# Kernel tuning notes

Hardware: AMD Instinct MI355X
Metric: run time of the kernel (lower is better)

Reference implementation:

```python
import jax, jax.numpy as jnp
import numpy as np

NQ, NKV, D = 32, 8, 64
HID = 2048
EPS = 1e-5
THETA = 1000000.0


def _rmsnorm(x, w):
    var = jnp.mean(x * x, axis=-1, keepdims=True)
    return x * jax.lax.rsqrt(var + EPS) * w


def setup_inputs() -> dict:
    key = jax.random.key(0)
    k1, k2, k3 = jax.random.split(key, 3)
    T = 2048
    positions = jnp.arange(T, dtype=jnp.int64) if jax.config.jax_enable_x64 else jnp.arange(T, dtype=jnp.int32)
    hidden_states = jax.random.normal(k1, (T, HID), dtype=jnp.float32)
    w_qkv = jax.random.normal(k2, (HID, (NQ + 2 * NKV) * D), dtype=jnp.float32) / np.sqrt(HID)
    w_out = jax.random.normal(k3, (NQ * D, HID), dtype=jnp.float32) / np.sqrt(NQ * D)
    q_ln_w = jnp.ones((D,), dtype=jnp.float32)
    k_ln_w = jnp.ones((D,), dtype=jnp.float32)
    return {"positions": positions, "hidden_states": hidden_states, "w_qkv": w_qkv,
            "w_out": w_out, "q_ln_w": q_ln_w, "k_ln_w": k_ln_w}


def reference(positions, hidden_states, w_qkv, w_out, q_ln_w, k_ln_w):
    T = hidden_states.shape[0]
    qkv = hidden_states @ w_qkv  # [T, (NQ+2*NKV)*D]
    q = qkv[:, : NQ * D].reshape(T, NQ, D)
    k = qkv[:, NQ * D : (NQ + NKV) * D].reshape(T, NKV, D)
    v = qkv[:, (NQ + NKV) * D :].reshape(T, NKV, D)
    # per-head RMSNorm on q and k
    q = _rmsnorm(q, q_ln_w)
    k = _rmsnorm(k, k_ln_w)
    # neox-style RoPE (rotate halves)
    inv_freq = 1.0 / (THETA ** (jnp.arange(0, D, 2, dtype=jnp.float32) / D))
    ang = positions.astype(jnp.float32)[:, None] * inv_freq  # [T, D/2]
    cos = jnp.cos(ang)[:, None, :]
    sin = jnp.sin(ang)[:, None, :]
    def rope(x):
        x1, x2 = x[..., : D // 2], x[..., D // 2 :]
        return jnp.concatenate([x1 * cos - x2 * sin, x2 * cos + x1 * sin], axis=-1)
    q = rope(q)
    k = rope(k)
    # grouped-query causal attention (one sequence, positions define order)
    G = NQ // NKV
    qg = q.reshape(T, NKV, G, D)
    scores = jnp.einsum('tkgd,skd->kgts', qg, k) * (D ** -0.5)  # [NKV,G,T,T]
    causal = jnp.arange(T)[:, None] >= jnp.arange(T)[None, :]
    scores = jnp.where(causal[None, None], scores, -1e30)
    probs = jax.nn.softmax(scores, axis=-1)
    attn = jnp.einsum('kgts,skd->tkgd', probs, v).reshape(T, NQ * D)
    return attn @ w_out
```

## Files before the change

### kernel.cpp

```cpp
#include <hip/hip_runtime.h>

typedef __bf16 bhalf;
typedef __bf16 bhalf8 __attribute__((ext_vector_type(8)));
typedef __bf16 bhalf4 __attribute__((ext_vector_type(4)));
typedef float f32x4 __attribute__((ext_vector_type(4)));

typedef __attribute__((address_space(1))) const void* gas_p;
typedef __attribute__((address_space(3))) void* las_p;

#define T_SEQ 2048
#define HIDN  2048
#define NQH   32
#define NKVH  8
#define DH    64
#define NQKV  3072

__global__ __launch_bounds__(256) void cast_bf16_k(const float* __restrict__ in,
                                                   bhalf* __restrict__ out, int n) {
  int i = (blockIdx.x * 256 + threadIdx.x) * 4;
  if (i + 3 < n) {
    float4 v = *(const float4*)(in + i);
    bhalf4 o;
    o[0] = (bhalf)v.x; o[1] = (bhalf)v.y; o[2] = (bhalf)v.z; o[3] = (bhalf)v.w;
    *(bhalf4*)(out + i) = o;
  }
}

__global__ __launch_bounds__(256) void transpose_cast64_k(const float* __restrict__ in,
                                                          bhalf* __restrict__ out,
                                                          int R, int C) {
  __shared__ bhalf tile[64][72];
  int tid = threadIdx.x;
  int bx = blockIdx.x * 64;
  int by = blockIdx.y * 64;
  int rl = tid >> 4, c4 = (tid & 15) * 4;
#pragma unroll
  for (int p = 0; p < 4; ++p) {
    float4 v = *(const float4*)(in + (size_t)(by + rl + 16 * p) * C + bx + c4);
    bhalf4 b;
    b[0] = (bhalf)v.x; b[1] = (bhalf)v.y; b[2] = (bhalf)v.z; b[3] = (bhalf)v.w;
    *(bhalf4*)&tile[rl + 16 * p][c4] = b;
  }
  __syncthreads();
  int c = tid >> 2, r0 = (tid & 3) * 16;
  bhalf8 o0, o1;
#pragma unroll
  for (int j = 0; j < 8; ++j) { o0[j] = tile[r0 + j][c]; o1[j] = tile[r0 + 8 + j][c]; }
  *(bhalf8*)(out + (size_t)(bx + c) * R + by + r0) = o0;
  *(bhalf8*)(out + (size_t)(bx + c) * R + by + r0 + 8) = o1;
}

__device__ __forceinline__ void gemm_core64(const bhalf* __restrict__ A,
                                            const bhalf* __restrict__ Bt,
                                            int Kstride, int Klen,
                                            int bm, int bn, int tid,
                                            bhalf* As, bhalf* Bs, f32x4 acc[4]) {
  int lane = tid & 63, wv = tid >> 6;
  int m16 = lane & 15, q4 = lane >> 4;
  int srow = tid >> 3;
  int scol = ((tid & 7) ^ (srow & 7)) * 8;
  const bhalf* asrc = A + (size_t)(bm + srow) * Kstride + scol;
  const bhalf* bsrc = Bt + (size_t)(bn + srow) * Kstride + scol;
  bhalf* adst = As + (wv * 8) * 64;
  bhalf* bdst = Bs + (wv * 8) * 64;
  int swz = m16 & 7;

  for (int k0 = 0; k0 < Klen; k0 += 64) {
#pragma unroll
    for (int c = 0; c < 2; ++c) {
      __builtin_amdgcn_global_load_lds((gas_p)(asrc + (size_t)(c * 32) * Kstride + k0),
                                       (las_p)(adst + c * 2048), 16, 0, 0);
      __builtin_amdgcn_global_load_lds((gas_p)(bsrc + (size_t)(c * 32) * Kstride + k0),
                                       (las_p)(bdst + c * 2048), 16, 0, 0);
    }
    __syncthreads();
    bhalf8 af[2], bf[4][2];
#pragma unroll
    for (int ks = 0; ks < 2; ++ks)
      af[ks] = *(const bhalf8*)&As[(wv * 16 + m16) * 64 + (((ks * 4 + q4) ^ swz) * 8)];
#pragma unroll
    for (int ni = 0; ni < 4; ++ni)
#pragma unroll
      for (int ks = 0; ks < 2; ++ks)
        bf[ni][ks] = *(const bhalf8*)&Bs[(ni * 16 + m16) * 64 + (((ks * 4 + q4) ^ swz) * 8)];
#pragma unroll
    for (int ni = 0; ni < 4; ++ni) {
      acc[ni] = __builtin_amdgcn_mfma_f32_16x16x32_bf16(af[0], bf[ni][0], acc[ni], 0, 0, 0);
      acc[ni] = __builtin_amdgcn_mfma_f32_16x16x32_bf16(af[1], bf[ni][1], acc[ni], 0, 0, 0);
    }
    __syncthreads();
  }
}

__global__ __launch_bounds__(256) void gemm1_fused_k(const bhalf* __restrict__ A,
                                                     const bhalf* __restrict__ Bt,
                                                     const int* __restrict__ pos,
                                                     const float* __restrict__ qw,
                                                     const float* __restrict__ kw,
                                                     bhalf* __restrict__ qo,
                                                     bhalf* __restrict__ ko,
                                                     bhalf* __restrict__ vt) {
  __shared__ __align__(16) bhalf As[64 * 64];
  __shared__ __align__(16) bhalf Bs[64 * 64];
  int tid = threadIdx.x, lane = tid & 63, wv = tid >> 6;
  int m16 = lane & 15, q4 = lane >> 4;
  int bm = blockIdx.y * 64, bn = blockIdx.x * 64, h = blockIdx.x;
  f32x4 zero4 = {0.f, 0.f, 0.f, 0.f};
  f32x4 acc[4];
#pragma unroll
  for (int ni = 0; ni < 4; ++ni) acc[ni] = zero4;

  gemm_core64(A, Bt, HIDN, HIDN, bm, bn, tid, As, Bs, acc);

  if (h < 40) {
    float wd[4];
    const float* wptr = (h < 32) ? qw : kw;
#pragma unroll
    for (int ni = 0; ni < 4; ++ni) wd[ni] = wptr[ni * 16 + m16];
    float f0 = exp2f((float)m16 * -0.6228615177913804f);
    float f1 = f0 * 0.001f;
#pragma unroll
    for (int r = 0; r < 4; ++r) {
      int trow = bm + wv * 16 + q4 * 4 + r;
      float x0 = acc[0][r], x1 = acc[1][r], x2 = acc[2][r], x3 = acc[3][r];
      float ss = x0 * x0 + x1 * x1 + x2 * x2 + x3 * x3;
      ss += __shfl_xor(ss, 1);
      ss += __shfl_xor(ss, 2);
      ss += __shfl_xor(ss, 4);
      ss += __shfl_xor(ss, 8);
      float sc = rsqrtf(ss * (1.0f / 64.0f) + 1e-5f);
      float y0 = x0 * sc * wd[0], y1 = x1 * sc * wd[1];
      float y2 = x2 * sc * wd[2], y3 = x3 * sc * wd[3];
      float p = (float)pos[trow];
      float a0 = p * f0, a1 = p * f1;
      float c0 = cosf(a0), s0 = sinf(a0), c1 = cosf(a1), s1 = sinf(a1);
      float o0 = y0 * c0 - y2 * s0, o2 = y2 * c0 + y0 * s0;
      float o1 = y1 * c1 - y3 * s1, o3 = y3 * c1 + y1 * s1;
      bhalf* dst = (h < 32) ? (qo + (size_t)trow * 2048 + h * 64 + m16)
                            : (ko + (size_t)trow * 512 + (h - 32) * 64 + m16);
      dst[0] = (bhalf)o0; dst[16] = (bhalf)o1; dst[32] = (bhalf)o2; dst[48] = (bhalf)o3;
    }
  } else {
#pragma unroll
    for (int r = 0; r < 4; ++r) {
      int trow = bm + wv * 16 + q4 * 4 + r;
#pragma unroll
      for (int ni = 0; ni < 4; ++ni)
        vt[(size_t)((h - 40) * 64 + ni * 16 + m16) * 2048 + trow] = (bhalf)acc[ni][r];
    }
  }
}

__global__ __launch_bounds__(256) void gemm2_k(const bhalf* __restrict__ A,
                                               const bhalf* __restrict__ Bt,
                                               float* __restrict__ Cpart) {
  __shared__ __align__(16) bhalf As[64 * 64];
  __shared__ __align__(16) bhalf Bs[64 * 64];
  int tid = threadIdx.x, lane = tid & 63, wv = tid >> 6;
  int m16 = lane & 15, q4 = lane >> 4;
  int bm = blockIdx.y * 64, bn = blockIdx.x * 64;
  int slice = blockIdx.z;
  f32x4 zero4 = {0.f, 0.f, 0.f, 0.f};
  f32x4 acc[4];
#pragma unroll
  for (int ni = 0; ni < 4; ++ni) acc[ni] = zero4;

  gemm_core64(A + slice * 1024, Bt + slice * 1024, HIDN, 1024, bm, bn, tid, As, Bs, acc);

  float* C = Cpart + (size_t)slice * (T_SEQ * HIDN);
#pragma unroll
  for (int r = 0; r < 4; ++r) {
    size_t base = (size_t)(bm + wv * 16 + q4 * 4 + r) * 2048 + bn + m16;
    C[base] = acc[0][r]; C[base + 16] = acc[1][r];
    C[base + 32] = acc[2][r]; C[base + 48] = acc[3][r];
  }
}

__global__ __launch_bounds__(256) void add2_k(const float* __restrict__ p0,
                                              const float* __restrict__ p1,
                                              float* __restrict__ out) {
  int i = (blockIdx.x * 256 + threadIdx.x) * 4;
  float4 a = *(const float4*)(p0 + i);
  float4 b = *(const float4*)(p1 + i);
  float4 o = {a.x + b.x, a.y + b.y, a.z + b.z, a.w + b.w};
  *(float4*)(out + i) = o;
}

__global__ __launch_bounds__(256) void attn_k(const bhalf* __restrict__ q,
                                              const bhalf* __restrict__ k,
                                              const bhalf* __restrict__ vt,
                                              bhalf* __restrict__ o) {
  __shared__ __align__(16) bhalf Kb[2][4096];
  __shared__ __align__(16) bhalf Vb[2][4096];
  __shared__ __align__(16) bhalf Pb[4][16][72];
  int tid = threadIdx.x, lane = tid & 63, w = tid >> 6;
  int h = blockIdx.x, kh = h >> 2;
  int qt = 31 - blockIdx.y;
  int qb = qt * 64;
  int m16 = lane & 15, q4 = lane >> 4;
  int wrow0 = qb + w * 16;

  const float C1 = 0.18033688011112042f;
  const float C2 = 11.541560327111707f;

  const bhalf* qp = q + (size_t)(wrow0 + m16) * 2048 + h * 64;
  bhalf8 qf0 = *(const bhalf8*)(qp + q4 * 8);
  bhalf8 qf1 = *(const bhalf8*)(qp + 32 + q4 * 8);

  int srow = tid >> 3;
  int scol = ((tid & 7) ^ (srow & 7)) * 8;
  const bhalf* ksrc = k + (size_t)srow * 512 + kh * 64 + scol;
  const bhalf* vsrc = vt + (size_t)(kh * 64 + srow) * 2048 + scol;
  bhalf* kdst = &Kb[0][0] + w * 512;
  bhalf* vdst = &Vb[0][0] + w * 512;

  auto stage = [&](int c) {
    int buf = c & 1, s0 = c * 64;
#pragma unroll
    for (int j = 0; j < 2; ++j) {
      __builtin_amdgcn_global_load_lds((gas_p)(ksrc + (size_t)(s0 + j * 32) * 512),
                                       (las_p)(kdst + buf * 4096 + j * 2048), 16, 0, 0);
      __builtin_amdgcn_global_load_lds((gas_p)(vsrc + (size_t)(j * 32) * 2048 + s0),
                                       (las_p)(vdst + buf * 4096 + j * 2048), 16, 0, 0);
    }
  };

  f32x4 zero4 = {0.f, 0.f, 0.f, 0.f};
  f32x4 oac[4];
  float psum[4] = {0.f, 0.f, 0.f, 0.f};
#pragma unroll
  for (int ni = 0; ni < 4; ++ni) oac[ni] = zero4;
  int swz = m16 & 7;

  stage(0);
  for (int c = 0; c <= qt; ++c) {
    __syncthreads();
    if (c < qt) stage(c + 1);
    int buf = c & 1, s0 = c * 64;
    if (c < qt) {
      bhalf8 kf[4][2];
#pragma unroll
      for (int st = 0; st < 4; ++st)
#pragma unroll
        for (int ks = 0; ks < 2; ++ks)
          kf[st][ks] = *(const bhalf8*)&Kb[buf][(st * 16 + m16) * 64 + (((ks * 4 + q4) ^ swz) * 8)];
      f32x4 sv[4];
#pragma unroll
      for (int st = 0; st < 4; ++st) {
        f32x4 t0 = __builtin_amdgcn_mfma_f32_16x16x32_bf16(qf0, kf[st][0], zero4, 0, 0, 0);
        sv[st] = __builtin_amdgcn_mfma_f32_16x16x32_bf16(qf1, kf[st][1], t0, 0, 0, 0);
      }
#pragma unroll
      for (int st = 0; st < 4; ++st)
#pragma unroll
        for (int r = 0; r < 4; ++r) {
          float pe = exp2f(sv[st][r] * C1 - C2);
          psum[r] += pe;
          Pb[w][q4 * 4 + r][st * 16 + m16] = (bhalf)pe;
        }
      bhalf8 vf[4][2];
#pragma unroll
      for (int ni = 0; ni < 4; ++ni)
#pragma unroll
        for (int ks = 0; ks < 2; ++ks)
          vf[ni][ks] = *(const bhalf8*)&Vb[buf][(ni * 16 + m16) * 64 + (((ks * 4 + q4) ^ swz) * 8)];
      bhalf8 ap0 = *(const bhalf8*)&Pb[w][m16][q4 * 8];
      bhalf8 ap1 = *(const bhalf8*)&Pb[w][m16][32 + q4 * 8];
#pragma unroll
      for (int ni = 0; ni < 4; ++ni) {
        oac[ni] = __builtin_amdgcn_mfma_f32_16x16x32_bf16(ap0, vf[ni][0], oac[ni], 0, 0, 0);
        oac[ni] = __builtin_amdgcn_mfma_f32_16x16x32_bf16(ap1, vf[ni][1], oac[ni], 0, 0, 0);
      }
    } else {
      bhalf8 kf[4][2];
      f32x4 sv[4];
#pragma unroll
      for (int st = 0; st < 4; ++st)
        if (st <= w) {
#pragma unroll
          for (int ks = 0; ks < 2; ++ks)
            kf[st][ks] = *(const bhalf8*)&Kb[buf][(st * 16 + m16) * 64 + (((ks * 4 + q4) ^ swz) * 8)];
          f32x4 t0 = __builtin_amdgcn_mfma_f32_16x16x32_bf16(qf0, kf[st][0], zero4, 0, 0, 0);
          sv[st] = __builtin_amdgcn_mfma_f32_16x16x32_bf16(qf1, kf[st][1], t0, 0, 0, 0);
        }
      int stwr = (w >= 2) ? 3 : 1;
#pragma unroll
      for (int st = 0; st < 4; ++st) {
        if (st > stwr) continue;
#pragma unroll
        for (int r = 0; r < 4; ++r) {
          float pe = 0.f;
          if (st <= w) {
            int trow = wrow0 + q4 * 4 + r;
            int col = s0 + st * 16 + m16;
            pe = (col <= trow) ? exp2f(sv[st][r] * C1 - C2) : 0.f;
          }
          psum[r] += pe;
          Pb[w][q4 * 4 + r][st * 16 + m16] = (bhalf)pe;
        }
      }
      int ksmax = (w >= 2) ? 1 : 0;
      bhalf8 vf[4][2];
#pragma unroll
      for (int ni = 0; ni < 4; ++ni)
#pragma unroll
        for (int ks = 0; ks < 2; ++ks)
          if (ks <= ksmax)
            vf[ni][ks] = *(const bhalf8*)&Vb[buf][(ni * 16 + m16) * 64 + (((ks * 4 + q4) ^ swz) * 8)];
      bhalf8 ap0 = *(const bhalf8*)&Pb[w][m16][q4 * 8];
#pragma unroll
      for (int ni = 0; ni < 4; ++ni)
        oac[ni] = __builtin_amdgcn_mfma_f32_16x16x32_bf16(ap0, vf[ni][0], oac[ni], 0, 0, 0);
      if (ksmax) {
        bhalf8 ap1 = *(const bhalf8*)&Pb[w][m16][32 + q4 * 8];
#pragma unroll
        for (int ni = 0; ni < 4; ++ni)
          oac[ni] = __builtin_amdgcn_mfma_f32_16x16x32_bf16(ap1, vf[ni][1], oac[ni], 0, 0, 0);
      }
    }
  }
#pragma unroll
  for (int r = 0; r < 4; ++r) {
    float ps = psum[r];
    ps += __shfl_xor(ps, 1);
    ps += __shfl_xor(ps, 2);
    ps += __shfl_xor(ps, 4);
    ps += __shfl_xor(ps, 8);
    psum[r] = 1.0f / ps;
  }
#pragma unroll
  for (int ni = 0; ni < 4; ++ni)
#pragma unroll
    for (int r = 0; r < 4; ++r) {
      int trow = wrow0 + q4 * 4 + r;
      o[(size_t)trow * 2048 + h * 64 + ni * 16 + m16] = (bhalf)(oac[ni][r] * psum[r]);
    }
}

extern "C" void kernel_launch(void* const* d_in, const int* in_sizes, int n_in,
                              void* d_out, int out_size, void* d_ws, size_t ws_size,
                              hipStream_t stream) {
  const int* positions = (const int*)d_in[0];
  const float* hidden  = (const float*)d_in[1];
  const float* w_qkv   = (const float*)d_in[2];
  const float* w_out   = (const float*)d_in[3];
  const float* q_ln    = (const float*)d_in[4];
  const float* k_ln    = (const float*)d_in[5];
  float* out = (float*)d_out;

  char* wsp = (char*)d_ws;
  bhalf* woutT   = (bhalf*)(wsp);
  bhalf* attn_bf = (bhalf*)(wsp + 8388608);
  float* part0   = (float*)(wsp + 16777216);
  float* part1   = (float*)(wsp + 33554432);
  bhalf* hid_bf  = (bhalf*)(wsp + 16777216);
  bhalf* wqkvT   = (bhalf*)(wsp + 25165824);
  bhalf* q_bf    = (bhalf*)(wsp + 50331648);
  bhalf* k_bf    = (bhalf*)(wsp + 58720256);
  bhalf* vt_g    = (bhalf*)(wsp + 60817408);

  cast_bf16_k<<<T_SEQ * HIDN / 1024, 256, 0, stream>>>(hidden, hid_bf, T_SEQ * HIDN);
  transpose_cast64_k<<<dim3(NQKV / 64, HIDN / 64), 256, 0, stream>>>(w_qkv, wqkvT, HIDN, NQKV);
  transpose_cast64_k<<<dim3(HIDN / 64, HIDN / 64), 256, 0, stream>>>(w_out, woutT, HIDN, HIDN);
  gemm1_fused_k<<<dim3(NQKV / 64, T_SEQ / 64), 256, 0, stream>>>(
      hid_bf, wqkvT, positions, q_ln, k_ln, q_bf, k_bf, vt_g);
  attn_k<<<dim3(NQH, 32), 256, 0, stream>>>(q_bf, k_bf, vt_g, attn_bf);
  gemm2_k<<<dim3(HIDN / 64, T_SEQ / 64, 2), 256, 0, stream>>>(attn_bf, woutT, part0);
  add2_k<<<T_SEQ * HIDN / 1024, 256, 0, stream>>>(part0, part1, out);
}
```

Baseline: 237.9 us.

## Double-buffer GEMM LDS tiles and grow M tile to 128 rows

The shared GEMM core now double-buffers the LDS tiles. It issues the async global-to-LDS loads for the next K step before computing the current one, which removes one barrier per iteration and overlaps memory traffic with MFMA work. Each block also covers 128 rows instead of 64, so each wave computes a 32x64 sub-tile that reuses its B fragments across two A fragments, and both GEMM grids are halved to match. This raises LDS use to 48 KB and doubles the accumulator registers, which may lower occupancy and halves the block count on a GPU with many CUs.

Result: faster. 233.0 us (-2.0%).

```diff
diff --git a/kernel.cpp b/kernel.cpp
--- a/kernel.cpp
+++ b/kernel.cpp
@@ -50,11 +50,11 @@
   *(bhalf8*)(out + (size_t)(bx + c) * R + by + r0 + 8) = o1;
 }
 
-__device__ __forceinline__ void gemm_core64(const bhalf* __restrict__ A,
-                                            const bhalf* __restrict__ Bt,
-                                            int Kstride, int Klen,
-                                            int bm, int bn, int tid,
-                                            bhalf* As, bhalf* Bs, f32x4 acc[4]) {
+__device__ __forceinline__ void gemm_core_db(const bhalf* __restrict__ A,
+                                             const bhalf* __restrict__ Bt,
+                                             int Kstride, int Klen,
+                                             int bm, int bn, int tid,
+                                             bhalf* As, bhalf* Bs, f32x4 acc[2][4]) {
   int lane = tid & 63, wv = tid >> 6;
   int m16 = lane & 15, q4 = lane >> 4;
   int srow = tid >> 3;
@@ -64,31 +64,46 @@
   bhalf* adst = As + (wv * 8) * 64;
   bhalf* bdst = Bs + (wv * 8) * 64;
   int swz = m16 & 7;
-
-  for (int k0 = 0; k0 < Klen; k0 += 64) {
-#pragma unroll
-    for (int c = 0; c < 2; ++c) {
+  int nit = Klen >> 6;
+
+  auto stage = [&](int it) {
+    int buf = it & 1, k0 = it * 64;
+#pragma unroll
+    for (int c = 0; c < 4; ++c)
       __builtin_amdgcn_global_load_lds((gas_p)(asrc + (size_t)(c * 32) * Kstride + k0),
-                                       (las_p)(adst + c * 2048), 16, 0, 0);
+                                       (las_p)(adst + buf * 8192 + c * 2048), 16, 0, 0);
+#pragma unroll
+    for (int c = 0; c < 2; ++c)
       __builtin_amdgcn_global_load_lds((gas_p)(bsrc + (size_t)(c * 32) * Kstride + k0),
-                                       (las_p)(bdst + c * 2048), 16, 0, 0);
-    }
+                                       (las_p)(bdst + buf * 4096 + c * 2048), 16, 0, 0);
+  };
+
+  stage(0);
+  for (int it = 0; it < nit; ++it) {
     __syncthreads();
-    bhalf8 af[2], bf[4][2];
-#pragma unroll
-    for (int ks = 0; ks < 2; ++ks)
-      af[ks] = *(const bhalf8*)&As[(wv * 16 + m16) * 64 + (((ks * 4 + q4) ^ swz) * 8)];
+    if (it + 1 < nit) stage(it + 1);
+    const bhalf* Ab = As + (it & 1) * 8192;
+    const bhalf* Bb = Bs + (it & 1) * 4096;
+    bhalf8 af[2][2], bf[4][2];
+#pragma unroll
+    for (int mi = 0; mi < 2; ++mi)
+#pragma unroll
+      for (int ks = 0; ks < 2; ++ks)
+        af[mi][ks] = *(const bhalf8*)&Ab[(wv * 32 + mi * 16 + m16) * 64 +
+                                         (((ks * 4 + q4) ^ swz) * 8)];
 #pragma unroll
     for (int ni = 0; ni < 4; ++ni)
 #pragma unroll
       for (int ks = 0; ks < 2; ++ks)
-        bf[ni][ks] = *(const bhalf8*)&Bs[(ni * 16 + m16) * 64 + (((ks * 4 + q4) ^ swz) * 8)];
-#pragma unroll
-    for (int ni = 0; ni < 4; ++ni) {
-      acc[ni] = __builtin_amdgcn_mfma_f32_16x16x32_bf16(af[0], bf[ni][0], acc[ni], 0, 0, 0);
-      acc[ni] = __builtin_amdgcn_mfma_f32_16x16x32_bf16(af[1], bf[ni][1], acc[ni], 0, 0, 0);
-    }
-    __syncthreads();
+        bf[ni][ks] = *(const bhalf8*)&Bb[(ni * 16 + m16) * 64 +
+                                         (((ks * 4 + q4) ^ swz) * 8)];
+#pragma unroll
+    for (int mi = 0; mi < 2; ++mi)
+#pragma unroll
+      for (int ni = 0; ni < 4; ++ni) {
+        acc[mi][ni] = __builtin_amdgcn_mfma_f32_16x16x32_bf16(af[mi][0], bf[ni][0], acc[mi][ni], 0, 0, 0);
+        acc[mi][ni] = __builtin_amdgcn_mfma_f32_16x16x32_bf16(af[mi][1], bf[ni][1], acc[mi][ni], 0, 0, 0);
+      }
   }
 }
 
@@ -100,17 +115,19 @@
                                                      bhalf* __restrict__ qo,
                                                      bhalf* __restrict__ ko,
                                                      bhalf* __restrict__ vt) {
-  __shared__ __align__(16) bhalf As[64 * 64];
-  __shared__ __align__(16) bhalf Bs[64 * 64];
+  __shared__ __align__(16) bhalf As[2 * 128 * 64];
+  __shared__ __align__(16) bhalf Bs[2 * 64 * 64];
   int tid = threadIdx.x, lane = tid & 63, wv = tid >> 6;
   int m16 = lane & 15, q4 = lane >> 4;
-  int bm = blockIdx.y * 64, bn = blockIdx.x * 64, h = blockIdx.x;
+  int bm = blockIdx.y * 128, bn = blockIdx.x * 64, h = blockIdx.x;
   f32x4 zero4 = {0.f, 0.f, 0.f, 0.f};
-  f32x4 acc[4];
-#pragma unroll
-  for (int ni = 0; ni < 4; ++ni) acc[ni] = zero4;
-
-  gemm_core64(A, Bt, HIDN, HIDN, bm, bn, tid, As, Bs, acc);
+  f32x4 acc[2][4];
+#pragma unroll
+  for (int mi = 0; mi < 2; ++mi)
+#pragma unroll
+    for (int ni = 0; ni < 4; ++ni) acc[mi][ni] = zero4;
+
+  gemm_core_db(A, Bt, HIDN, HIDN, bm, bn, tid, As, Bs, acc);
 
   if (h < 40) {
     float wd[4];
@@ -120,60 +137,68 @@
     float f0 = exp2f((float)m16 * -0.6228615177913804f);
     float f1 = f0 * 0.001f;
 #pragma unroll
-    for (int r = 0; r < 4; ++r) {
-      int trow = bm + wv * 16 + q4 * 4 + r;
-      float x0 = acc[0][r], x1 = acc[1][r], x2 = acc[2][r], x3 = acc[3][r];
-      float ss = x0 * x0 + x1 * x1 + x2 * x2 + x3 * x3;
-      ss += __shfl_xor(ss, 1);
-      ss += __shfl_xor(ss, 2);
-      ss += __shfl_xor(ss, 4);
-      ss += __shfl_xor(ss, 8);
-      float sc = rsqrtf(ss * (1.0f / 64.0f) + 1e-5f);
-      float y0 = x0 * sc * wd[0], y1 = x1 * sc * wd[1];
-      float y2 = x2 * sc * wd[2], y3 = x3 * sc * wd[3];
-      float p = (float)pos[trow];
-      float a0 = p * f0, a1 = p * f1;
-      float c0 = cosf(a0), s0 = sinf(a0), c1 = cosf(a1), s1 = sinf(a1);
-      float o0 = y0 * c0 - y2 * s0, o2 = y2 * c0 + y0 * s0;
-      float o1 = y1 * c1 - y3 * s1, o3 = y3 * c1 + y1 * s1;
-      bhalf* dst = (h < 32) ? (qo + (size_t)trow * 2048 + h * 64 + m16)
-                            : (ko + (size_t)trow * 512 + (h - 32) * 64 + m16);
-      dst[0] = (bhalf)o0; dst[16] = (bhalf)o1; dst[32] = (bhalf)o2; dst[48] = (bhalf)o3;
-    }
+    for (int mi = 0; mi < 2; ++mi)
+#pragma unroll
+      for (int r = 0; r < 4; ++r) {
+        int trow = bm + wv * 32 + mi * 16 + q4 * 4 + r;
+        float x0 = acc[mi][0][r], x1 = acc[mi][1][r], x2 = acc[mi][2][r], x3 = acc[mi][3][r];
+        float ss = x0 * x0 + x1 * x1 + x2 * x2 + x3 * x3;
+        ss += __shfl_xor(ss, 1);
+        ss += __shfl_xor(ss, 2);
+        ss += __shfl_xor(ss, 4);
+        ss += __shfl_xor(ss, 8);
+        float sc = rsqrtf(ss * (1.0f / 64.0f) + 1e-5f);
+        float y0 = x0 * sc * wd[0], y1 = x1 * sc * wd[1];
+        float y2 = x2 * sc * wd[2], y3 = x3 * sc * wd[3];
+        float p = (float)pos[trow];
+        float a0 = p * f0, a1 = p * f1;
+        float c0 = cosf(a0), s0 = sinf(a0), c1 = cosf(a1), s1 = sinf(a1);
+        float o0 = y0 * c0 - y2 * s0, o2 = y2 * c0 + y0 * s0;
+        float o1 = y1 * c1 - y3 * s1, o3 = y3 * c1 + y1 * s1;
+        bhalf* dst = (h < 32) ? (qo + (size_t)trow * 2048 + h * 64 + m16)
+                              : (ko + (size_t)trow * 512 + (h - 32) * 64 + m16);
+        dst[0] = (bhalf)o0; dst[16] = (bhalf)o1; dst[32] = (bhalf)o2; dst[48] = (bhalf)o3;
+      }
   } else {
 #pragma unroll
-    for (int r = 0; r < 4; ++r) {
-      int trow = bm + wv * 16 + q4 * 4 + r;
-#pragma unroll
-      for (int ni = 0; ni < 4; ++ni)
-        vt[(size_t)((h - 40) * 64 + ni * 16 + m16) * 2048 + trow] = (bhalf)acc[ni][r];
-    }
+    for (int mi = 0; mi < 2; ++mi)
+#pragma unroll
+      for (int r = 0; r < 4; ++r) {
+        int trow = bm + wv * 32 + mi * 16 + q4 * 4 + r;
+#pragma unroll
+        for (int ni = 0; ni < 4; ++ni)
+          vt[(size_t)((h - 40) * 64 + ni * 16 + m16) * 2048 + trow] = (bhalf)acc[mi][ni][r];
+      }
   }
 }
 
 __global__ __launch_bounds__(256) void gemm2_k(const bhalf* __restrict__ A,
                                                const bhalf* __restrict__ Bt,
                                                float* __restrict__ Cpart) {
-  __shared__ __align__(16) bhalf As[64 * 64];
-  __shared__ __align__(16) bhalf Bs[64 * 64];
+  __shared__ __align__(16) bhalf As[2 * 128 * 64];
+  __shared__ __align__(16) bhalf Bs[2 * 64 * 64];
   int tid = threadIdx.x, lane = tid & 63, wv = tid >> 6;
   int m16 = lane & 15, q4 = lane >> 4;
-  int bm = blockIdx.y * 64, bn = blockIdx.x * 64;
+  int bm = blockIdx.y * 128, bn = blockIdx.x * 64;
   int slice = blockIdx.z;
   f32x4 zero4 = {0.f, 0.f, 0.f, 0.f};
-  f32x4 acc[4];
-#pragma unroll
-  for (int ni = 0; ni < 4; ++ni) acc[ni] = zero4;
-
-  gemm_core64(A + slice * 1024, Bt + slice * 1024, HIDN, 1024, bm, bn, tid, As, Bs, acc);
+  f32x4 acc[2][4];
+#pragma unroll
+  for (int mi = 0; mi < 2; ++mi)
+#pragma unroll
+    for (int ni = 0; ni < 4; ++ni) acc[mi][ni] = zero4;
+
+  gemm_core_db(A + slice * 1024, Bt + slice * 1024, HIDN, 1024, bm, bn, tid, As, Bs, acc);
 
   float* C = Cpart + (size_t)slice * (T_SEQ * HIDN);
 #pragma unroll
-  for (int r = 0; r < 4; ++r) {
-    size_t base = (size_t)(bm + wv * 16 + q4 * 4 + r) * 2048 + bn + m16;
-    C[base] = acc[0][r]; C[base + 16] = acc[1][r];
-    C[base + 32] = acc[2][r]; C[base + 48] = acc[3][r];
-  }
+  for (int mi = 0; mi < 2; ++mi)
+#pragma unroll
+    for (int r = 0; r < 4; ++r) {
+      size_t base = (size_t)(bm + wv * 32 + mi * 16 + q4 * 4 + r) * 2048 + bn + m16;
+      C[base] = acc[mi][0][r]; C[base + 16] = acc[mi][1][r];
+      C[base + 32] = acc[mi][2][r]; C[base + 48] = acc[mi][3][r];
+    }
 }
 
 __global__ __launch_bounds__(256) void add2_k(const float* __restrict__ p0,
@@ -362,9 +387,9 @@
   cast_bf16_k<<<T_SEQ * HIDN / 1024, 256, 0, stream>>>(hidden, hid_bf, T_SEQ * HIDN);
   transpose_cast64_k<<<dim3(NQKV / 64, HIDN / 64), 256, 0, stream>>>(w_qkv, wqkvT, HIDN, NQKV);
   transpose_cast64_k<<<dim3(HIDN / 64, HIDN / 64), 256, 0, stream>>>(w_out, woutT, HIDN, HIDN);
-  gemm1_fused_k<<<dim3(NQKV / 64, T_SEQ / 64), 256, 0, stream>>>(
+  gemm1_fused_k<<<dim3(NQKV / 64, T_SEQ / 128), 256, 0, stream>>>(
       hid_bf, wqkvT, positions, q_ln, k_ln, q_bf, k_bf, vt_g);
   attn_k<<<dim3(NQH, 32), 256, 0, stream>>>(q_bf, k_bf, vt_g, attn_bf);
-  gemm2_k<<<dim3(HIDN / 64, T_SEQ / 64, 2), 256, 0, stream>>>(attn_bf, woutT, part0);
+  gemm2_k<<<dim3(HIDN / 64, T_SEQ / 128, 2), 256, 0, stream>>>(attn_bf, woutT, part0);
   add2_k<<<T_SEQ * HIDN / 1024, 256, 0, stream>>>(part0, part1, out);
 }
```

## Switch GEMMs to 32x32x16 MFMA with 64x128 tiles and fragment-ordered LDS

Applied to the files above, without the earlier changes.

Replaces the 16x16x32 MFMA GEMM core with a 32x32x16 variant. Each workgroup now computes a 64x128 tile, with each wave producing a 32x64 output. LDS is laid out in MFMA fragment order so each lane loads its fragment contiguously, which removes the XOR swizzle. The fused RMSNorm/RoPE epilogue and the output stores are rewritten for the 32x32 accumulator layout, where one head spans two accumulators per wave. The aim is fewer MFMA instructions and LDS reads per FLOP and better operand reuse, at the cost of fewer workgroups and higher register pressure.

Result: slower. 295.7 us (+24.3%).

```diff
diff --git a/kernel.cpp b/kernel.cpp
--- a/kernel.cpp
+++ b/kernel.cpp
@@ -4,6 +4,7 @@
 typedef __bf16 bhalf8 __attribute__((ext_vector_type(8)));
 typedef __bf16 bhalf4 __attribute__((ext_vector_type(4)));
 typedef float f32x4 __attribute__((ext_vector_type(4)));
+typedef float f32x16 __attribute__((ext_vector_type(16)));
 
 typedef __attribute__((address_space(1))) const void* gas_p;
 typedef __attribute__((address_space(3))) void* las_p;
@@ -50,43 +51,43 @@
   *(bhalf8*)(out + (size_t)(bx + c) * R + by + r0 + 8) = o1;
 }
 
-__device__ __forceinline__ void gemm_core64(const bhalf* __restrict__ A,
+__device__ __forceinline__ void gemm_core32(const bhalf* __restrict__ A,
                                             const bhalf* __restrict__ Bt,
-                                            int Kstride, int Klen,
-                                            int bm, int bn, int tid,
-                                            bhalf* As, bhalf* Bs, f32x4 acc[4]) {
+                                            int K, int Klen, int bm, int bn, int tid,
+                                            bhalf* As, bhalf* Bs, f32x16 acc[2]) {
   int lane = tid & 63, wv = tid >> 6;
-  int m16 = lane & 15, q4 = lane >> 4;
-  int srow = tid >> 3;
-  int scol = ((tid & 7) ^ (srow & 7)) * 8;
-  const bhalf* asrc = A + (size_t)(bm + srow) * Kstride + scol;
-  const bhalf* bsrc = Bt + (size_t)(bn + srow) * Kstride + scol;
-  bhalf* adst = As + (wv * 8) * 64;
-  bhalf* bdst = Bs + (wv * 8) * 64;
-  int swz = m16 & 7;
+  int r32 = lane & 31, khi = (lane >> 5) * 8;
+  const bhalf* ag[2];
+  const bhalf* bg[4];
+#pragma unroll
+  for (int i = 0; i < 2; ++i) {
+    int a = 2 * wv + i;
+    ag[i] = A + (size_t)(bm + (a >> 2) * 32 + r32) * K + (a & 3) * 16 + khi;
+  }
+#pragma unroll
+  for (int j = 0; j < 4; ++j) {
+    int b = 4 * wv + j;
+    bg[j] = Bt + (size_t)(bn + (b >> 2) * 32 + r32) * K + (b & 3) * 16 + khi;
+  }
+  bhalf* adst = As + (2 * wv) * 512;
+  bhalf* bdst = Bs + (4 * wv) * 512;
+  int mt = wv >> 1, ntb = (wv & 1) * 2;
 
   for (int k0 = 0; k0 < Klen; k0 += 64) {
 #pragma unroll
-    for (int c = 0; c < 2; ++c) {
-      __builtin_amdgcn_global_load_lds((gas_p)(asrc + (size_t)(c * 32) * Kstride + k0),
-                                       (las_p)(adst + c * 2048), 16, 0, 0);
-      __builtin_amdgcn_global_load_lds((gas_p)(bsrc + (size_t)(c * 32) * Kstride + k0),
-                                       (las_p)(bdst + c * 2048), 16, 0, 0);
-    }
+    for (int i = 0; i < 2; ++i)
+      __builtin_amdgcn_global_load_lds((gas_p)(ag[i] + k0), (las_p)(adst + i * 512), 16, 0, 0);
+#pragma unroll
+    for (int j = 0; j < 4; ++j)
+      __builtin_amdgcn_global_load_lds((gas_p)(bg[j] + k0), (las_p)(bdst + j * 512), 16, 0, 0);
     __syncthreads();
-    bhalf8 af[2], bf[4][2];
-#pragma unroll
-    for (int ks = 0; ks < 2; ++ks)
-      af[ks] = *(const bhalf8*)&As[(wv * 16 + m16) * 64 + (((ks * 4 + q4) ^ swz) * 8)];
-#pragma unroll
-    for (int ni = 0; ni < 4; ++ni)
-#pragma unroll
-      for (int ks = 0; ks < 2; ++ks)
-        bf[ni][ks] = *(const bhalf8*)&Bs[(ni * 16 + m16) * 64 + (((ks * 4 + q4) ^ swz) * 8)];
-#pragma unroll
-    for (int ni = 0; ni < 4; ++ni) {
-      acc[ni] = __builtin_amdgcn_mfma_f32_16x16x32_bf16(af[0], bf[ni][0], acc[ni], 0, 0, 0);
-      acc[ni] = __builtin_amdgcn_mfma_f32_16x16x32_bf16(af[1], bf[ni][1], acc[ni], 0, 0, 0);
+#pragma unroll
+    for (int ks = 0; ks < 4; ++ks) {
+      bhalf8 af  = *(const bhalf8*)&As[(mt * 4 + ks) * 512 + lane * 8];
+      bhalf8 bf0 = *(const bhalf8*)&Bs[(ntb * 4 + ks) * 512 + lane * 8];
+      bhalf8 bf1 = *(const bhalf8*)&Bs[((ntb + 1) * 4 + ks) * 512 + lane * 8];
+      acc[0] = __builtin_amdgcn_mfma_f32_32x32x16_bf16(af, bf0, acc[0], 0, 0, 0);
+      acc[1] = __builtin_amdgcn_mfma_f32_32x32x16_bf16(af, bf1, acc[1], 0, 0, 0);
     }
     __syncthreads();
   }
@@ -100,53 +101,55 @@
                                                      bhalf* __restrict__ qo,
                                                      bhalf* __restrict__ ko,
                                                      bhalf* __restrict__ vt) {
-  __shared__ __align__(16) bhalf As[64 * 64];
-  __shared__ __align__(16) bhalf Bs[64 * 64];
+  __shared__ __align__(16) bhalf As[8 * 512];
+  __shared__ __align__(16) bhalf Bs[16 * 512];
   int tid = threadIdx.x, lane = tid & 63, wv = tid >> 6;
-  int m16 = lane & 15, q4 = lane >> 4;
-  int bm = blockIdx.y * 64, bn = blockIdx.x * 64, h = blockIdx.x;
-  f32x4 zero4 = {0.f, 0.f, 0.f, 0.f};
-  f32x4 acc[4];
-#pragma unroll
-  for (int ni = 0; ni < 4; ++ni) acc[ni] = zero4;
-
-  gemm_core64(A, Bt, HIDN, HIDN, bm, bn, tid, As, Bs, acc);
-
-  if (h < 40) {
-    float wd[4];
-    const float* wptr = (h < 32) ? qw : kw;
-#pragma unroll
-    for (int ni = 0; ni < 4; ++ni) wd[ni] = wptr[ni * 16 + m16];
-    float f0 = exp2f((float)m16 * -0.6228615177913804f);
-    float f1 = f0 * 0.001f;
-#pragma unroll
-    for (int r = 0; r < 4; ++r) {
-      int trow = bm + wv * 16 + q4 * 4 + r;
-      float x0 = acc[0][r], x1 = acc[1][r], x2 = acc[2][r], x3 = acc[3][r];
-      float ss = x0 * x0 + x1 * x1 + x2 * x2 + x3 * x3;
+  int r32 = lane & 31;
+  int bm = blockIdx.y * 64, bn = blockIdx.x * 128;
+  f32x16 acc[2];
+#pragma unroll
+  for (int r = 0; r < 16; ++r) { acc[0][r] = 0.f; acc[1][r] = 0.f; }
+
+  gemm_core32(A, Bt, HIDN, HIDN, bm, bn, tid, As, Bs, acc);
+
+  int hh = blockIdx.x * 2 + (wv & 1);
+  int wm = (wv >> 1) * 32;
+  int rhi = 4 * (lane >> 5);
+  if (hh < 40) {
+    const float* wptr = (hh < 32) ? qw : kw;
+    float w0 = wptr[r32], w1 = wptr[r32 + 32];
+    float f0 = exp2f((float)r32 * -0.6228615177913804f);
+#pragma unroll
+    for (int r = 0; r < 16; ++r) {
+      int row = (r & 3) + 8 * (r >> 2) + rhi;
+      int trow = bm + wm + row;
+      float x0 = acc[0][r], x1 = acc[1][r];
+      float ss = x0 * x0 + x1 * x1;
       ss += __shfl_xor(ss, 1);
       ss += __shfl_xor(ss, 2);
       ss += __shfl_xor(ss, 4);
       ss += __shfl_xor(ss, 8);
+      ss += __shfl_xor(ss, 16);
       float sc = rsqrtf(ss * (1.0f / 64.0f) + 1e-5f);
-      float y0 = x0 * sc * wd[0], y1 = x1 * sc * wd[1];
-      float y2 = x2 * sc * wd[2], y3 = x3 * sc * wd[3];
-      float p = (float)pos[trow];
-      float a0 = p * f0, a1 = p * f1;
-      float c0 = cosf(a0), s0 = sinf(a0), c1 = cosf(a1), s1 = sinf(a1);
-      float o0 = y0 * c0 - y2 * s0, o2 = y2 * c0 + y0 * s0;
-      float o1 = y1 * c1 - y3 * s1, o3 = y3 * c1 + y1 * s1;
-      bhalf* dst = (h < 32) ? (qo + (size_t)trow * 2048 + h * 64 + m16)
-                            : (ko + (size_t)trow * 512 + (h - 32) * 64 + m16);
-      dst[0] = (bhalf)o0; dst[16] = (bhalf)o1; dst[32] = (bhalf)o2; dst[48] = (bhalf)o3;
+      float y0 = x0 * sc * w0, y1 = x1 * sc * w1;
+      float ang = (float)pos[trow] * f0;
+      float c = cosf(ang), s = sinf(ang);
+      float o0 = y0 * c - y1 * s, o1 = y1 * c + y0 * s;
+      if (hh < 32) {
+        bhalf* dst = qo + (size_t)trow * 2048 + hh * 64 + r32;
+        dst[0] = (bhalf)o0; dst[32] = (bhalf)o1;
+      } else {
+        bhalf* dst = ko + (size_t)trow * 512 + (hh - 32) * 64 + r32;
+        dst[0] = (bhalf)o0; dst[32] = (bhalf)o1;
+      }
     }
   } else {
 #pragma unroll
-    for (int r = 0; r < 4; ++r) {
-      int trow = bm + wv * 16 + q4 * 4 + r;
-#pragma unroll
-      for (int ni = 0; ni < 4; ++ni)
-        vt[(size_t)((h - 40) * 64 + ni * 16 + m16) * 2048 + trow] = (bhalf)acc[ni][r];
+    for (int r = 0; r < 16; ++r) {
+      int row = (r & 3) + 8 * (r >> 2) + rhi;
+      int trow = bm + wm + row;
+      vt[(size_t)((hh - 40) * 64 + r32) * 2048 + trow] = (bhalf)acc[0][r];
+      vt[(size_t)((hh - 40) * 64 + r32 + 32) * 2048 + trow] = (bhalf)acc[1][r];
     }
   }
 }
@@ -154,25 +157,27 @@
 __global__ __launch_bounds__(256) void gemm2_k(const bhalf* __restrict__ A,
                                                const bhalf* __restrict__ Bt,
                                                float* __restrict__ Cpart) {
-  __shared__ __align__(16) bhalf As[64 * 64];
-  __shared__ __align__(16) bhalf Bs[64 * 64];
+  __shared__ __align__(16) bhalf As[8 * 512];
+  __shared__ __align__(16) bhalf Bs[16 * 512];
   int tid = threadIdx.x, lane = tid & 63, wv = tid >> 6;
-  int m16 = lane & 15, q4 = lane >> 4;
-  int bm = blockIdx.y * 64, bn = blockIdx.x * 64;
+  int r32 = lane & 31;
+  int bm = blockIdx.y * 64, bn = blockIdx.x * 128;
   int slice = blockIdx.z;
-  f32x4 zero4 = {0.f, 0.f, 0.f, 0.f};
-  f32x4 acc[4];
-#pragma unroll
-  for (int ni = 0; ni < 4; ++ni) acc[ni] = zero4;
-
-  gemm_core64(A + slice * 1024, Bt + slice * 1024, HIDN, 1024, bm, bn, tid, As, Bs, acc);
+  f32x16 acc[2];
+#pragma unroll
+  for (int r = 0; r < 16; ++r) { acc[0][r] = 0.f; acc[1][r] = 0.f; }
+
+  gemm_core32(A + slice * 1024, Bt + slice * 1024, HIDN, 1024, bm, bn, tid, As, Bs, acc);
 
   float* C = Cpart + (size_t)slice * (T_SEQ * HIDN);
-#pragma unroll
-  for (int r = 0; r < 4; ++r) {
-    size_t base = (size_t)(bm + wv * 16 + q4 * 4 + r) * 2048 + bn + m16;
-    C[base] = acc[0][r]; C[base + 16] = acc[1][r];
-    C[base + 32] = acc[2][r]; C[base + 48] = acc[3][r];
+  int wm = (wv >> 1) * 32, wn = (wv & 1) * 64;
+  int rhi = 4 * (lane >> 5);
+#pragma unroll
+  for (int r = 0; r < 16; ++r) {
+    int row = (r & 3) + 8 * (r >> 2) + rhi;
+    size_t base = (size_t)(bm + wm + row) * 2048 + bn + wn + r32;
+    C[base] = acc[0][r];
+    C[base + 32] = acc[1][r];
   }
 }
 
@@ -362,9 +367,9 @@
   cast_bf16_k<<<T_SEQ * HIDN / 1024, 256, 0, stream>>>(hidden, hid_bf, T_SEQ * HIDN);
   transpose_cast64_k<<<dim3(NQKV / 64, HIDN / 64), 256, 0, stream>>>(w_qkv, wqkvT, HIDN, NQKV);
   transpose_cast64_k<<<dim3(HIDN / 64, HIDN / 64), 256, 0, stream>>>(w_out, woutT, HIDN, HIDN);
-  gemm1_fused_k<<<dim3(NQKV / 64, T_SEQ / 64), 256, 0, stream>>>(
+  gemm1_fused_k<<<dim3(NQKV / 128, T_SEQ / 64), 256, 0, stream>>>(
       hid_bf, wqkvT, positions, q_ln, k_ln, q_bf, k_bf, vt_g);
   attn_k<<<dim3(NQH, 32), 256, 0, stream>>>(q_bf, k_bf, vt_g, attn_bf);
-  gemm2_k<<<dim3(HIDN / 64, T_SEQ / 64, 2), 256, 0, stream>>>(attn_bf, woutT, part0);
+  gemm2_k<<<dim3(HIDN / 128, T_SEQ / 64, 2), 256, 0, stream>>>(attn_bf, woutT, part0);
   add2_k<<<T_SEQ * HIDN / 1024, 256, 0, stream>>>(part0, part1, out);
 }
```
